# Optimization experiments

Hardware: AMD Instinct MI355X
Metric: run time of the kernel (lower is better)

The kernel has to match this reference:

```python
import jax, jax.numpy as jnp
import numpy as np
import math

FANO_LINES = [(0,1,2),(0,3,4),(0,6,5),(1,3,5),(1,4,6),(2,3,6),(2,5,4)]
WINDOW = 16

def fano_mask(T: int) -> jnp.ndarray:
    """[7,T,T] bool mask: head h attends to j if (j%7 in line_h and j<=i) or i-WINDOW<=j<=i."""
    membership = np.zeros((7, 7), dtype=bool)
    for h, line in enumerate(FANO_LINES):
        membership[h, list(line)] = True
    j = np.arange(T)
    fano = membership[:, j % 7]                      # [7,T]
    i = j[:, None]
    causal = (j[None, :] <= i)                       # [T,T]
    local = causal & (j[None, :] >= i - WINDOW)      # [T,T]
    mask = (fano[:, None, :] & causal[None]) | local[None]
    return jnp.asarray(mask)

def setup_inputs() -> dict:
    key = jax.random.key(0)
    ks = jax.random.split(key, 5)
    B, T, D = 1, 4096, 896
    s = 1.0 / math.sqrt(D)
    return {
        "x":  jax.random.normal(ks[0], (B, T, D), dtype=jnp.float32),
        "Wq": jax.random.normal(ks[1], (D, D), dtype=jnp.float32) * s,
        "Wk": jax.random.normal(ks[2], (D, D), dtype=jnp.float32) * s,
        "Wv": jax.random.normal(ks[3], (D, D), dtype=jnp.float32) * s,
        "Wo": jax.random.normal(ks[4], (D, D), dtype=jnp.float32) * s,
    }

def reference(x, Wq, Wk, Wv, Wo):
    B, T, D = x.shape
    H = 7
    hd = D // H
    # torch Linear: x @ W.T
    q = (x @ Wq.T).reshape(B, T, H, hd)
    k = (x @ Wk.T).reshape(B, T, H, hd)
    v = (x @ Wv.T).reshape(B, T, H, hd)
    scale = 1.0 / math.sqrt(hd)
    scores = jnp.einsum('bthc,bshc->bhts', q, k) * scale   # [B,7,T,T]
    mask = fano_mask(T)                                    # [7,T,T]
    neg = jnp.asarray(-jnp.inf, dtype=scores.dtype)
    scores = jnp.where(mask[None], scores, neg)
    attn = jax.nn.softmax(scores, axis=-1)
    out = jnp.einsum('bhts,bshc->bthc', attn, v).reshape(B, T, D)
    return out @ Wo.T
```

## Files before the change

### kernel.cpp

```cpp
#include <hip/hip_runtime.h>
#include <stdint.h>

typedef unsigned short ushort_t;
typedef __bf16 bf16x8 __attribute__((ext_vector_type(8)));
typedef __bf16 bf16x2 __attribute__((ext_vector_type(2)));
typedef float f32x4 __attribute__((ext_vector_type(4)));
typedef float f32x16 __attribute__((ext_vector_type(16)));

#define T_SEQ 4096
#define D_MODEL 896
#define CHUNKS_PER_BLOCK 4
#define MAXSPLIT 8

#define LSK 136
#define LSV 72

__constant__ int d_LINEMASK[7] = {0x07, 0x19, 0x61, 0x2A, 0x52, 0x4C, 0x34};
__constant__ int d_R[7][3] = {{0,1,2},{0,3,4},{0,5,6},{1,3,5},{1,4,6},{2,3,6},{2,4,5}};

__device__ inline unsigned f2bf(float f) {
    unsigned x = __float_as_uint(f);
    return (x + 0x7fffu + ((x >> 16) & 1u)) >> 16;
}
__device__ inline float lo_f(unsigned x) { return __uint_as_float(x << 16); }
__device__ inline float hi_f(unsigned x) { return __uint_as_float(x & 0xFFFF0000u); }

__device__ __forceinline__ unsigned pk_bf2(float lo, float hi) {
    union { bf16x2 h; unsigned u; } cv;
    cv.h = (bf16x2){(__bf16)lo, (__bf16)hi};
    return cv.u;
}

__host__ __device__ inline int nsplit_of(int t) {
    int a = (192 * t + 189) / 7 + 3;
    int nch_ub = (a + 63) >> 6;
    return (nch_ub + 2 + CHUNKS_PER_BLOCK - 1) / CHUNKS_PER_BLOCK;
}

__global__ __launch_bounds__(256)
void cvt5(const float* __restrict__ x,  const float* __restrict__ wq,
          const float* __restrict__ wk, const float* __restrict__ wv,
          const float* __restrict__ wo,
          ushort_t* __restrict__ xb,  ushort_t* __restrict__ wqb,
          ushort_t* __restrict__ wkb, ushort_t* __restrict__ wvb,
          ushort_t* __restrict__ wob) {
    const int ten = blockIdx.y;
    const float* s = (ten == 0) ? x : (ten == 1) ? wq : (ten == 2) ? wk
                   : (ten == 3) ? wv : wo;
    ushort_t* d = (ten == 0) ? xb : (ten == 1) ? wqb : (ten == 2) ? wkb
                : (ten == 3) ? wvb : wob;
    const int n8 = ((ten == 0) ? T_SEQ * D_MODEL : D_MODEL * D_MODEL) >> 3;
    for (int i = blockIdx.x * 256 + threadIdx.x; i < n8; i += gridDim.x * 256) {
        float4 a = ((const float4*)s)[2 * i];
        float4 b = ((const float4*)s)[2 * i + 1];
        uint4 u;
        u.x = f2bf(a.x) | (f2bf(a.y) << 16);
        u.y = f2bf(a.z) | (f2bf(a.w) << 16);
        u.z = f2bf(b.x) | (f2bf(b.y) << 16);
        u.w = f2bf(b.z) | (f2bf(b.w) << 16);
        ((uint4*)d)[i] = u;
    }
}

__device__ __forceinline__ void async_cp16(const void* g, void* l) {
    __builtin_amdgcn_global_load_lds(
        (__attribute__((address_space(1))) void*)g,
        (__attribute__((address_space(3))) void*)l,
        16, 0, 0);
}

template <bool C32>
__global__ __launch_bounds__(256)
void gemm_nt_dma(const ushort_t* __restrict__ A,
                 const ushort_t* __restrict__ B0,
                 const ushort_t* __restrict__ B1,
                 const ushort_t* __restrict__ B2,
                 void* __restrict__ C0,
                 void* __restrict__ C1,
                 void* __restrict__ C2) {
    const int z = blockIdx.z;
    const ushort_t* B = (z == 0) ? B0 : (z == 1) ? B1 : B2;
    void* C = (z == 0) ? C0 : (z == 1) ? C1 : C2;

    const int K = D_MODEL, N = D_MODEL;
    const int i0 = blockIdx.x * 128;
    const int n0 = blockIdx.y * 128;

    __shared__ __align__(16) ushort_t As[128 * 32];
    __shared__ __align__(16) ushort_t Bs[128 * 32];

    const int t = threadIdx.x;
    const int w = t >> 6, lane = t & 63;
    const int wm = (w >> 1) * 64, wn = (w & 1) * 64;
    const int lr = lane & 15, lq = lane >> 4;

    const int srow = w * 16 + (lane >> 2);
    const int scol = (lane & 3) * 8;
    const ushort_t* gA0 = A + (size_t)(i0 + srow) * K + scol;
    const ushort_t* gA1 = A + (size_t)(i0 + 64 + srow) * K + scol;
    const ushort_t* gB0 = B + (size_t)(n0 + srow) * K + scol;
    const ushort_t* gB1 = B + (size_t)(n0 + 64 + srow) * K + scol;
    ushort_t* lA0 = &As[(w * 16) * 32];
    ushort_t* lA1 = &As[(64 + w * 16) * 32];
    ushort_t* lB0 = &Bs[(w * 16) * 32];
    ushort_t* lB1 = &Bs[(64 + w * 16) * 32];

    f32x4 acc[4][4];
#pragma unroll
    for (int a = 0; a < 4; a++)
#pragma unroll
        for (int b = 0; b < 4; b++) acc[a][b] = (f32x4){0.f, 0.f, 0.f, 0.f};

    for (int k0 = 0; k0 < K; k0 += 32) {
        __syncthreads();
        async_cp16(gA0 + k0, lA0);
        async_cp16(gA1 + k0, lA1);
        async_cp16(gB0 + k0, lB0);
        async_cp16(gB1 + k0, lB1);
        __builtin_amdgcn_s_waitcnt(0);
        __syncthreads();

        bf16x8 af[4], bfr[4];
#pragma unroll
        for (int mi = 0; mi < 4; mi++)
            af[mi] = *(const bf16x8*)&As[(wm + mi * 16 + lr) * 32 + lq * 8];
#pragma unroll
        for (int ni = 0; ni < 4; ni++)
            bfr[ni] = *(const bf16x8*)&Bs[(wn + ni * 16 + lr) * 32 + lq * 8];
#pragma unroll
        for (int mi = 0; mi < 4; mi++)
#pragma unroll
            for (int ni = 0; ni < 4; ni++)
                acc[mi][ni] = __builtin_amdgcn_mfma_f32_16x16x32_bf16(
                    af[mi], bfr[ni], acc[mi][ni], 0, 0, 0);
    }

    if (C32) {
        float* Cf = (float*)C;
#pragma unroll
        for (int mi = 0; mi < 4; mi++)
#pragma unroll
            for (int ni = 0; ni < 4; ni++)
#pragma unroll
                for (int r = 0; r < 4; r++) {
                    int row = i0 + wm + mi * 16 + lq * 4 + r;
                    int col = n0 + wn + ni * 16 + lr;
                    Cf[(size_t)row * N + col] = acc[mi][ni][r];
                }
    } else {
        ushort_t* Cb = (ushort_t*)C;
#pragma unroll
        for (int mi = 0; mi < 4; mi++)
#pragma unroll
            for (int ni = 0; ni < 4; ni++)
#pragma unroll
                for (int r = 0; r < 4; r++) {
                    int row = i0 + wm + mi * 16 + lq * 4 + r;
                    int col = n0 + wn + ni * 16 + lr;
                    Cb[(size_t)row * N + col] = (ushort_t)f2bf(acc[mi][ni][r]);
                }
    }
}

__device__ inline void vt_scatter8(ushort_t* vtcol, uint4 vv) {
    vtcol[0 * LSV] = (ushort_t)(vv.x & 0xFFFFu);
    vtcol[1 * LSV] = (ushort_t)(vv.x >> 16);
    vtcol[2 * LSV] = (ushort_t)(vv.y & 0xFFFFu);
    vtcol[3 * LSV] = (ushort_t)(vv.y >> 16);
    vtcol[4 * LSV] = (ushort_t)(vv.z & 0xFFFFu);
    vtcol[5 * LSV] = (ushort_t)(vv.z >> 16);
    vtcol[6 * LSV] = (ushort_t)(vv.w & 0xFFFFu);
    vtcol[7 * LSV] = (ushort_t)(vv.w >> 16);
}

__device__ inline int jof(int p, int r0, int r1, int r2) {
    int g = p / 3, rs = p - 3 * g;
    return 7 * g + ((rs == 0) ? r0 : (rs == 1) ? r1 : r2);
}

__device__ __forceinline__ void issue_kv(const ushort_t* __restrict__ Kb,
                                         const ushort_t* __restrict__ Vb,
                                         int j, int h, int dim0,
                                         uint4 kreg[4], uint4 vreg[4]) {
    if (j >= 0 && j < T_SEQ) {
        const ushort_t* kp = Kb + (size_t)j * D_MODEL + h * 128 + dim0;
        const ushort_t* vp = Vb + (size_t)j * D_MODEL + h * 128 + dim0;
#pragma unroll
        for (int v = 0; v < 4; v++) {
            kreg[v] = *(const uint4*)(kp + v * 8);
            vreg[v] = *(const uint4*)(vp + v * 8);
        }
    } else {
        uint4 zz = {0u, 0u, 0u, 0u};
#pragma unroll
        for (int v = 0; v < 4; v++) { kreg[v] = zz; vreg[v] = zz; }
    }
}

__device__ __forceinline__ void write_kv(ushort_t* Ks, ushort_t* Vt,
                                         int kk, int dim0,
                                         const uint4 kreg[4], const uint4 vreg[4]) {
#pragma unroll
    for (int v = 0; v < 4; v++) {
        *(uint4*)&Ks[kk * LSK + dim0 + v * 8] = kreg[v];
        vt_scatter8(&Vt[(dim0 + v * 8) * LSV + kk], vreg[v]);
    }
}

__global__ __launch_bounds__(256, 2)
void fano_attn_split(const ushort_t* __restrict__ Qb,
                     const ushort_t* __restrict__ Kb,
                     const ushort_t* __restrict__ Vb,
                     ushort_t* __restrict__ Opart,
                     float* __restrict__ Lm) {
    const int h = blockIdx.y;
    const int p = (int)gridDim.x - 1 - (int)blockIdx.x;

    int tile = 63, pbase0 = 0;
    for (int u = 0; u < 64; ++u) {
        int s = nsplit_of(u);
        if (p < pbase0 + s) { tile = u; break; }
        pbase0 += s;
    }
    const int sp = p - pbase0;
    const int Sloc = nsplit_of(tile);

    const int i0 = tile * 64;
    const int t = threadIdx.x;
    const int w = t >> 6, lane = t & 63;
    const int wq = w >> 1, wk = w & 1;
    const int q = lane & 31;
    const int hl = lane >> 5;
    const int iq = i0 + wq * 32 + q;

    __shared__ __align__(16) ushort_t Ks[2][64 * LSK];
    __shared__ __align__(16) ushort_t Vt[2][128 * LSV];

    const int lm = d_LINEMASK[h];
    const int r0 = d_R[h][0], r1 = d_R[h][1], r2 = d_R[h][2];
    const float scale = 0.08838834764831845f;

    bf16x8 qf[8];
    {
        const ushort_t* qrow = Qb + (size_t)iq * D_MODEL + h * 128;
#pragma unroll
        for (int f = 0; f < 8; f++)
            qf[f] = *(const bf16x8*)(qrow + f * 16 + hl * 8);
    }

    f32x16 O[4];
#pragma unroll
    for (int d4 = 0; d4 < 4; d4++)
#pragma unroll
        for (int e = 0; e < 16; e++) O[d4][e] = 0.f;
    float m = -1e30f;
    float l = 0.f;

    const int imax = i0 + 63;
    const int ncomp = (imax - r0) / 7 + (imax - r1) / 7 + (imax - r2) / 7 + 3;
    const int nch = (ncomp + 63) >> 6;
    const int ntot = nch + 2;
    const int cstart = (sp * ntot) / Sloc;
    const int cend = ((sp + 1) * ntot) / Sloc;

    auto chunk_j = [&](int cc) -> int {
        if (cc >= nch) {
            const int jbase = (cc == nch) ? i0 - 16 : i0 + 48;
            return jbase + lane;
        }
        return jof(cc * 64 + lane, r0, r1, r2);
    };

    uint4 kreg[4], vreg[4];
    if (cstart < cend) {
        issue_kv(Kb, Vb, chunk_j(cstart), h, w * 32, kreg, vreg);
        write_kv(Ks[0], Vt[0], lane, w * 32, kreg, vreg);
        if (cstart + 1 < cend)
            issue_kv(Kb, Vb, chunk_j(cstart + 1), h, w * 32, kreg, vreg);
    }
    __syncthreads();
    int cur = 0;

    for (int cc = cstart; cc < cend; cc++) {
        const bool band = (cc >= nch);
        const int jbase = (cc == nch) ? i0 - 16 : i0 + 48;

        if (cc + 1 < cend)
            write_kv(Ks[cur ^ 1], Vt[cur ^ 1], lane, w * 32, kreg, vreg);
        if (cc + 2 < cend)
            issue_kv(Kb, Vb, chunk_j(cc + 2), h, w * 32, kreg, vreg);

        int jmin = band ? jbase : jof(cc * 64, r0, r1, r2);
        if (jmin <= i0 + wq * 32 + 31) {
            const ushort_t* KsC = Ks[cur];
            const ushort_t* VtC = Vt[cur];

            f32x16 S;
#pragma unroll
            for (int e = 0; e < 16; e++) S[e] = 0.f;
#pragma unroll
            for (int f = 0; f < 8; f++) {
                bf16x8 kf = *(const bf16x8*)
                    &KsC[(wk * 32 + q) * LSK + f * 16 + hl * 8];
                S = __builtin_amdgcn_mfma_f32_32x32x16_bf16(kf, qf[f], S, 0, 0, 0);
            }

            const bool interior = !band && (jof(cc * 64 + 63, r0, r1, r2) <= i0 + wq * 32);
            if (interior) {
#pragma unroll
                for (int e = 0; e < 16; e++) S[e] *= scale;
            } else if (band) {
#pragma unroll
                for (int g4 = 0; g4 < 4; g4++) {
                    int j0 = jbase + wk * 32 + 8 * g4 + 4 * hl;
#pragma unroll
                    for (int e = 0; e < 4; e++) {
                        int j = j0 + e;
                        int jm = ((j % 7) + 7) % 7;
                        bool ok = (j >= 0) && !((lm >> jm) & 1) &&
                                  (j <= iq) && (j >= iq - 16);
                        S[g4 * 4 + e] = ok ? S[g4 * 4 + e] * scale : -1e30f;
                    }
                }
            } else {
#pragma unroll
                for (int g4 = 0; g4 < 4; g4++) {
                    int p0 = cc * 64 + wk * 32 + 8 * g4 + 4 * hl;
                    int g = p0 / 3, rs = p0 - 3 * g;
#pragma unroll
                    for (int e = 0; e < 4; e++) {
                        int j = 7 * g + ((rs == 0) ? r0 : (rs == 1) ? r1 : r2);
                        S[g4 * 4 + e] = (j <= iq) ? S[g4 * 4 + e] * scale : -1e30f;
                        if (++rs == 3) { rs = 0; ++g; }
                    }
                }
            }

            float cm = -1e30f;
#pragma unroll
            for (int e = 0; e < 16; e++) cm = fmaxf(cm, S[e]);
            cm = fmaxf(cm, __shfl_xor(cm, 32));

            const bool defer = __all(cm <= m && m >= -60.f);
            float mn, a = 1.f;
            if (defer) {
                mn = m;
            } else {
                mn = fmaxf(fmaxf(m, cm), -60.f);
                a = __expf(m - mn);
                m = mn;
            }
            float rs_ = 0.f;
#pragma unroll
            for (int e = 0; e < 16; e++) {
                S[e] = __expf(S[e] - mn);
                rs_ += S[e];
            }
            rs_ += __shfl_xor(rs_, 32);
            if (defer) {
                l = l + rs_;
            } else {
                l = l * a + rs_;
#pragma unroll
                for (int d4 = 0; d4 < 4; d4++)
#pragma unroll
                    for (int e = 0; e < 16; e++) O[d4][e] *= a;
            }

            bf16x8 pf[2];
#pragma unroll
            for (int f = 0; f < 2; f++) {
                unsigned lo0 = pk_bf2(S[8 * f + 0], S[8 * f + 1]);
                unsigned lo1 = pk_bf2(S[8 * f + 2], S[8 * f + 3]);
                unsigned hi0 = pk_bf2(S[8 * f + 4], S[8 * f + 5]);
                unsigned hi1 = pk_bf2(S[8 * f + 6], S[8 * f + 7]);
                unsigned s0 = hl ? lo0 : hi0;
                unsigned s1 = hl ? lo1 : hi1;
                unsigned rv0 = __shfl_xor(s0, 32);
                unsigned rv1 = __shfl_xor(s1, 32);
                uint4 tw;
                tw.x = hl ? rv0 : lo0;
                tw.y = hl ? rv1 : lo1;
                tw.z = hl ? hi0 : rv0;
                tw.w = hl ? hi1 : rv1;
                pf[f] = *(const bf16x8*)&tw;
            }

#pragma unroll
            for (int d4 = 0; d4 < 4; d4++) {
#pragma unroll
                for (int f = 0; f < 2; f++) {
                    bf16x8 vf = *(const bf16x8*)
                        &VtC[(d4 * 32 + q) * LSV + wk * 32 + f * 16 + hl * 8];
                    O[d4] = __builtin_amdgcn_mfma_f32_32x32x16_bf16(vf, pf[f], O[d4], 0, 0, 0);
                }
            }
        }

        __syncthreads();
        cur ^= 1;
    }

    float* sc = (float*)&Ks[0][0];
    float* mlsc = (float*)&Vt[0][0];
    if (wk == 1) {
#pragma unroll
        for (int d4 = 0; d4 < 4; d4++)
#pragma unroll
            for (int e = 0; e < 16; e++) {
                int d = d4 * 32 + (e & 3) + 8 * (e >> 2) + 4 * hl;
                sc[((size_t)wq * 128 + d) * 32 + q] = O[d4][e];
            }
        if (hl == 0) {
            mlsc[(wq * 32 + q) * 2 + 0] = m;
            mlsc[(wq * 32 + q) * 2 + 1] = l;
        }
    }
    __syncthreads();
    if (wk == 0) {
        float m1 = mlsc[(wq * 32 + q) * 2 + 0];
        float l1 = mlsc[(wq * 32 + q) * 2 + 1];
        float mm = fmaxf(m, m1);
        float a0 = __expf(m - mm), a1 = __expf(m1 - mm);
        float lL = l * a0 + l1 * a1;

        const size_t pbase = ((size_t)p * 7 + h) * 64;
        const int row = wq * 32 + q;
#pragma unroll
        for (int d4 = 0; d4 < 4; d4++)
#pragma unroll
            for (int rg = 0; rg < 4; rg++) {
                float v0_, v1_, v2_, v3_;
                {
                    int e = rg * 4;
                    int dA = d4 * 32 + 8 * rg + 4 * hl;
                    v0_ = O[d4][e + 0] * a0 + sc[((size_t)wq * 128 + dA + 0) * 32 + q] * a1;
                    v1_ = O[d4][e + 1] * a0 + sc[((size_t)wq * 128 + dA + 1) * 32 + q] * a1;
                    v2_ = O[d4][e + 2] * a0 + sc[((size_t)wq * 128 + dA + 2) * 32 + q] * a1;
                    v3_ = O[d4][e + 3] * a0 + sc[((size_t)wq * 128 + dA + 3) * 32 + q] * a1;
                }
                uint2 u;
                u.x = pk_bf2(v0_, v1_);
                u.y = pk_bf2(v2_, v3_);
                *(uint2*)&Opart[(pbase + row) * 128 + d4 * 32 + 8 * rg + 4 * hl] = u;
            }
        if (hl == 0) {
            Lm[(pbase + row) * 2 + 0] = mm;
            Lm[(pbase + row) * 2 + 1] = lL;
        }
    }
}

__global__ __launch_bounds__(256)
void attn_merge(const ushort_t* __restrict__ Opart,
                const float* __restrict__ Lm,
                ushort_t* __restrict__ Ab) {
    const int h = blockIdx.y;
    const int tt = blockIdx.x;
    int pb = 0;
    for (int u = 0; u < tt; ++u) pb += nsplit_of(u);
    const int S = nsplit_of(tt);
    const int lrow = threadIdx.x >> 2;
    const int row = tt * 64 + lrow;
    const int d0 = (threadIdx.x & 3) * 32;

    float ms[MAXSPLIT], ls[MAXSPLIT], M = -1e30f;
#pragma unroll
    for (int s = 0; s < MAXSPLIT; s++) {
        ms[s] = -1e30f;
        ls[s] = 0.f;
        if (s < S) {
            size_t q = (((size_t)(pb + s) * 7 + h) * 64 + lrow) * 2;
            ms[s] = Lm[q];
            ls[s] = Lm[q + 1];
        }
        M = fmaxf(M, ms[s]);
    }
    float L = 0.f, c[MAXSPLIT];
#pragma unroll
    for (int s = 0; s < MAXSPLIT; s++) {
        c[s] = __expf(ms[s] - M);
        L += c[s] * ls[s];
    }
    float acc[32];
#pragma unroll
    for (int k = 0; k < 32; k++) acc[k] = 0.f;
#pragma unroll
    for (int s = 0; s < MAXSPLIT; s++) {
        if (s < S) {
            const float cs = c[s];
            const ushort_t* op =
                Opart + (((size_t)(pb + s) * 7 + h) * 64 + lrow) * 128 + d0;
#pragma unroll
            for (int v = 0; v < 4; v++) {
                uint4 u = *(const uint4*)(op + v * 8);
                acc[v * 8 + 0] += cs * lo_f(u.x);
                acc[v * 8 + 1] += cs * hi_f(u.x);
                acc[v * 8 + 2] += cs * lo_f(u.y);
                acc[v * 8 + 3] += cs * hi_f(u.y);
                acc[v * 8 + 4] += cs * lo_f(u.z);
                acc[v * 8 + 5] += cs * hi_f(u.z);
                acc[v * 8 + 6] += cs * lo_f(u.w);
                acc[v * 8 + 7] += cs * hi_f(u.w);
            }
        }
    }
    float invL = 1.f / L;
    ushort_t* dst = Ab + (size_t)row * D_MODEL + h * 128 + d0;
#pragma unroll
    for (int v = 0; v < 4; v++) {
        uint4 u;
        u.x = f2bf(acc[v * 8 + 0] * invL) | (f2bf(acc[v * 8 + 1] * invL) << 16);
        u.y = f2bf(acc[v * 8 + 2] * invL) | (f2bf(acc[v * 8 + 3] * invL) << 16);
        u.z = f2bf(acc[v * 8 + 4] * invL) | (f2bf(acc[v * 8 + 5] * invL) << 16);
        u.w = f2bf(acc[v * 8 + 6] * invL) | (f2bf(acc[v * 8 + 7] * invL) << 16);
        *(uint4*)(dst + v * 8) = u;
    }
}

extern "C" void kernel_launch(void* const* d_in, const int* in_sizes, int n_in,
                              void* d_out, int out_size, void* d_ws, size_t ws_size,
                              hipStream_t stream) {
    const float* x  = (const float*)d_in[0];
    const float* Wq = (const float*)d_in[1];
    const float* Wk = (const float*)d_in[2];
    const float* Wv = (const float*)d_in[3];
    const float* Wo = (const float*)d_in[4];

    int NP = 0;
    for (int u = 0; u < 64; ++u) NP += nsplit_of(u);

    const size_t n  = (size_t)T_SEQ * D_MODEL;
    const size_t nw = (size_t)D_MODEL * D_MODEL;
    ushort_t* xb  = (ushort_t*)d_ws + 128;
    ushort_t* Wqb = xb + n;
    ushort_t* Wkb = Wqb + nw;
    ushort_t* Wvb = Wkb + nw;
    ushort_t* Wob = Wvb + nw;
    ushort_t* Qb  = Wob + nw;
    ushort_t* Kb  = Qb + n;
    ushort_t* Vb  = Kb + n;
    ushort_t* Ab  = Vb + n;
    ushort_t* Opart = Ab + n;
    float*    Lm  = (float*)(Opart + (size_t)NP * 7 * 64 * 128);

    cvt5<<<dim3(1792, 5), 256, 0, stream>>>(x, Wq, Wk, Wv, Wo,
                                            xb, Wqb, Wkb, Wvb, Wob);
    gemm_nt_dma<false><<<dim3(32, 7, 3), 256, 0, stream>>>(
        xb, Wqb, Wkb, Wvb, Qb, Kb, Vb);
    fano_attn_split<<<dim3(NP, 7), 256, 0, stream>>>(
        Qb, Kb, Vb, Opart, Lm);
    attn_merge<<<dim3(64, 7), 256, 0, stream>>>(Opart, Lm, Ab);
    gemm_nt_dma<true><<<dim3(32, 7, 1), 256, 0, stream>>>(
        Ab, Wob, Wob, Wob, d_out, d_out, d_out);
}
```

Before: 147.1 us.

## Single-buffer K/V shared memory to double attention kernel occupancy

Replaces the double-buffered K/V shared-memory tiles with a single buffer and raises launch bounds from 2 to 4 blocks per CU. The prefetch distance drops from two chunks to one, and each iteration now uses two barriers around the shared-memory write. The goal is to hide latency with more resident blocks instead of in-block double buffering. In exchange it adds synchronisation per chunk and tighter register limits, which could cause spills with the large O accumulators.

```diff
diff --git a/kernel.cpp b/kernel.cpp
--- a/kernel.cpp
+++ b/kernel.cpp
@@ -207,7 +207,7 @@
     }
 }
 
-__global__ __launch_bounds__(256, 2)
+__global__ __launch_bounds__(256, 4)
 void fano_attn_split(const ushort_t* __restrict__ Qb,
                      const ushort_t* __restrict__ Kb,
                      const ushort_t* __restrict__ Vb,
@@ -233,8 +233,9 @@
     const int hl = lane >> 5;
     const int iq = i0 + wq * 32 + q;
 
-    __shared__ __align__(16) ushort_t Ks[2][64 * LSK];
-    __shared__ __align__(16) ushort_t Vt[2][128 * LSV];
+    __shared__ __align__(16) ushort_t smem[64 * LSK + 128 * LSV];
+    ushort_t* Ks = smem;
+    ushort_t* Vt = smem + 64 * LSK;
 
     const int lm = d_LINEMASK[h];
     const int r0 = d_R[h][0], r1 = d_R[h][1], r2 = d_R[h][2];
@@ -272,137 +273,130 @@
     };
 
     uint4 kreg[4], vreg[4];
-    if (cstart < cend) {
+    if (cstart < cend)
         issue_kv(Kb, Vb, chunk_j(cstart), h, w * 32, kreg, vreg);
-        write_kv(Ks[0], Vt[0], lane, w * 32, kreg, vreg);
-        if (cstart + 1 < cend)
-            issue_kv(Kb, Vb, chunk_j(cstart + 1), h, w * 32, kreg, vreg);
-    }
-    __syncthreads();
-    int cur = 0;
 
     for (int cc = cstart; cc < cend; cc++) {
         const bool band = (cc >= nch);
         const int jbase = (cc == nch) ? i0 - 16 : i0 + 48;
 
+        __syncthreads();
+        write_kv(Ks, Vt, lane, w * 32, kreg, vreg);
+        __syncthreads();
+
         if (cc + 1 < cend)
-            write_kv(Ks[cur ^ 1], Vt[cur ^ 1], lane, w * 32, kreg, vreg);
-        if (cc + 2 < cend)
-            issue_kv(Kb, Vb, chunk_j(cc + 2), h, w * 32, kreg, vreg);
-
-        int jmin = band ? jbase : jof(cc * 64, r0, r1, r2);
-        if (jmin <= i0 + wq * 32 + 31) {
-            const ushort_t* KsC = Ks[cur];
-            const ushort_t* VtC = Vt[cur];
-
-            f32x16 S;
-#pragma unroll
-            for (int e = 0; e < 16; e++) S[e] = 0.f;
-#pragma unroll
-            for (int f = 0; f < 8; f++) {
-                bf16x8 kf = *(const bf16x8*)
-                    &KsC[(wk * 32 + q) * LSK + f * 16 + hl * 8];
-                S = __builtin_amdgcn_mfma_f32_32x32x16_bf16(kf, qf[f], S, 0, 0, 0);
-            }
-
-            const bool interior = !band && (jof(cc * 64 + 63, r0, r1, r2) <= i0 + wq * 32);
-            if (interior) {
-#pragma unroll
-                for (int e = 0; e < 16; e++) S[e] *= scale;
-            } else if (band) {
-#pragma unroll
-                for (int g4 = 0; g4 < 4; g4++) {
-                    int j0 = jbase + wk * 32 + 8 * g4 + 4 * hl;
-#pragma unroll
-                    for (int e = 0; e < 4; e++) {
-                        int j = j0 + e;
-                        int jm = ((j % 7) + 7) % 7;
-                        bool ok = (j >= 0) && !((lm >> jm) & 1) &&
-                                  (j <= iq) && (j >= iq - 16);
-                        S[g4 * 4 + e] = ok ? S[g4 * 4 + e] * scale : -1e30f;
-                    }
-                }
-            } else {
-#pragma unroll
-                for (int g4 = 0; g4 < 4; g4++) {
-                    int p0 = cc * 64 + wk * 32 + 8 * g4 + 4 * hl;
-                    int g = p0 / 3, rs = p0 - 3 * g;
-#pragma unroll
-                    for (int e = 0; e < 4; e++) {
-                        int j = 7 * g + ((rs == 0) ? r0 : (rs == 1) ? r1 : r2);
-                        S[g4 * 4 + e] = (j <= iq) ? S[g4 * 4 + e] * scale : -1e30f;
-                        if (++rs == 3) { rs = 0; ++g; }
-                    }
+            issue_kv(Kb, Vb, chunk_j(cc + 1), h, w * 32, kreg, vreg);
+
+        {
+            int jmin = band ? jbase : jof(cc * 64, r0, r1, r2);
+            if (jmin > i0 + wq * 32 + 31) continue;
+        }
+
+        f32x16 S;
+#pragma unroll
+        for (int e = 0; e < 16; e++) S[e] = 0.f;
+#pragma unroll
+        for (int f = 0; f < 8; f++) {
+            bf16x8 kf = *(const bf16x8*)
+                &Ks[(wk * 32 + q) * LSK + f * 16 + hl * 8];
+            S = __builtin_amdgcn_mfma_f32_32x32x16_bf16(kf, qf[f], S, 0, 0, 0);
+        }
+
+        const bool interior = !band && (jof(cc * 64 + 63, r0, r1, r2) <= i0 + wq * 32);
+        if (interior) {
+#pragma unroll
+            for (int e = 0; e < 16; e++) S[e] *= scale;
+        } else if (band) {
+#pragma unroll
+            for (int g4 = 0; g4 < 4; g4++) {
+                int j0 = jbase + wk * 32 + 8 * g4 + 4 * hl;
+#pragma unroll
+                for (int e = 0; e < 4; e++) {
+                    int j = j0 + e;
+                    int jm = ((j % 7) + 7) % 7;
+                    bool ok = (j >= 0) && !((lm >> jm) & 1) &&
+                              (j <= iq) && (j >= iq - 16);
+                    S[g4 * 4 + e] = ok ? S[g4 * 4 + e] * scale : -1e30f;
                 }
             }
-
-            float cm = -1e30f;
-#pragma unroll
-            for (int e = 0; e < 16; e++) cm = fmaxf(cm, S[e]);
-            cm = fmaxf(cm, __shfl_xor(cm, 32));
-
-            const bool defer = __all(cm <= m && m >= -60.f);
-            float mn, a = 1.f;
-            if (defer) {
-                mn = m;
-            } else {
-                mn = fmaxf(fmaxf(m, cm), -60.f);
-                a = __expf(m - mn);
-                m = mn;
-            }
-            float rs_ = 0.f;
-#pragma unroll
-            for (int e = 0; e < 16; e++) {
-                S[e] = __expf(S[e] - mn);
-                rs_ += S[e];
-            }
-            rs_ += __shfl_xor(rs_, 32);
-            if (defer) {
-                l = l + rs_;
-            } else {
-                l = l * a + rs_;
-#pragma unroll
-                for (int d4 = 0; d4 < 4; d4++)
-#pragma unroll
-                    for (int e = 0; e < 16; e++) O[d4][e] *= a;
-            }
-
-            bf16x8 pf[2];
-#pragma unroll
-            for (int f = 0; f < 2; f++) {
-                unsigned lo0 = pk_bf2(S[8 * f + 0], S[8 * f + 1]);
-                unsigned lo1 = pk_bf2(S[8 * f + 2], S[8 * f + 3]);
-                unsigned hi0 = pk_bf2(S[8 * f + 4], S[8 * f + 5]);
-                unsigned hi1 = pk_bf2(S[8 * f + 6], S[8 * f + 7]);
-                unsigned s0 = hl ? lo0 : hi0;
-                unsigned s1 = hl ? lo1 : hi1;
-                unsigned rv0 = __shfl_xor(s0, 32);
-                unsigned rv1 = __shfl_xor(s1, 32);
-                uint4 tw;
-                tw.x = hl ? rv0 : lo0;
-                tw.y = hl ? rv1 : lo1;
-                tw.z = hl ? hi0 : rv0;
-                tw.w = hl ? hi1 : rv1;
-                pf[f] = *(const bf16x8*)&tw;
-            }
-
-#pragma unroll
-            for (int d4 = 0; d4 < 4; d4++) {
-#pragma unroll
-                for (int f = 0; f < 2; f++) {
-                    bf16x8 vf = *(const bf16x8*)
-                        &VtC[(d4 * 32 + q) * LSV + wk * 32 + f * 16 + hl * 8];
-                    O[d4] = __builtin_amdgcn_mfma_f32_32x32x16_bf16(vf, pf[f], O[d4], 0, 0, 0);
+        } else {
+#pragma unroll
+            for (int g4 = 0; g4 < 4; g4++) {
+                int p0 = cc * 64 + wk * 32 + 8 * g4 + 4 * hl;
+                int g = p0 / 3, rs = p0 - 3 * g;
+#pragma unroll
+                for (int e = 0; e < 4; e++) {
+                    int j = 7 * g + ((rs == 0) ? r0 : (rs == 1) ? r1 : r2);
+                    S[g4 * 4 + e] = (j <= iq) ? S[g4 * 4 + e] * scale : -1e30f;
+                    if (++rs == 3) { rs = 0; ++g; }
                 }
             }
         }
 
-        __syncthreads();
-        cur ^= 1;
-    }
-
-    float* sc = (float*)&Ks[0][0];
-    float* mlsc = (float*)&Vt[0][0];
+        float cm = -1e30f;
+#pragma unroll
+        for (int e = 0; e < 16; e++) cm = fmaxf(cm, S[e]);
+        cm = fmaxf(cm, __shfl_xor(cm, 32));
+
+        const bool defer = __all(cm <= m && m >= -60.f);
+        float mn, a = 1.f;
+        if (defer) {
+            mn = m;
+        } else {
+            mn = fmaxf(fmaxf(m, cm), -60.f);
+            a = __expf(m - mn);
+            m = mn;
+        }
+        float rs_ = 0.f;
+#pragma unroll
+        for (int e = 0; e < 16; e++) {
+            S[e] = __expf(S[e] - mn);
+            rs_ += S[e];
+        }
+        rs_ += __shfl_xor(rs_, 32);
+        if (defer) {
+            l = l + rs_;
+        } else {
+            l = l * a + rs_;
+#pragma unroll
+            for (int d4 = 0; d4 < 4; d4++)
+#pragma unroll
+                for (int e = 0; e < 16; e++) O[d4][e] *= a;
+        }
+
+        bf16x8 pf[2];
+#pragma unroll
+        for (int f = 0; f < 2; f++) {
+            unsigned lo0 = pk_bf2(S[8 * f + 0], S[8 * f + 1]);
+            unsigned lo1 = pk_bf2(S[8 * f + 2], S[8 * f + 3]);
+            unsigned hi0 = pk_bf2(S[8 * f + 4], S[8 * f + 5]);
+            unsigned hi1 = pk_bf2(S[8 * f + 6], S[8 * f + 7]);
+            unsigned s0 = hl ? lo0 : hi0;
+            unsigned s1 = hl ? lo1 : hi1;
+            unsigned rv0 = __shfl_xor(s0, 32);
+            unsigned rv1 = __shfl_xor(s1, 32);
+            uint4 tw;
+            tw.x = hl ? rv0 : lo0;
+            tw.y = hl ? rv1 : lo1;
+            tw.z = hl ? hi0 : rv0;
+            tw.w = hl ? hi1 : rv1;
+            pf[f] = *(const bf16x8*)&tw;
+        }
+
+#pragma unroll
+        for (int d4 = 0; d4 < 4; d4++) {
+#pragma unroll
+            for (int f = 0; f < 2; f++) {
+                bf16x8 vf = *(const bf16x8*)
+                    &Vt[(d4 * 32 + q) * LSV + wk * 32 + f * 16 + hl * 8];
+                O[d4] = __builtin_amdgcn_mfma_f32_32x32x16_bf16(vf, pf[f], O[d4], 0, 0, 0);
+            }
+        }
+    }
+
+    __syncthreads();
+    float* sc = (float*)smem;
+    float* mlsc = (float*)(smem + 16384);
     if (wk == 1) {
 #pragma unroll
         for (int d4 = 0; d4 < 4; d4++)
```

New measurement: 585.4 us, median of 2. +297.8%, slower.
